# Performance work log

Measured on AMD Instinct MI355X. Metric: run time of the kernel, lower is better.

## Reference

```python
import jax, jax.numpy as jnp
import numpy as np

N_NODES = 50000
N_EDGES = 800000
D = 128
N_REL = 237


def _layer(x, W_I, W_O, rel, b, src, dst):
    # messages over real edges: compose (sub) then project
    msg = (x[src] - rel[edge_safe(dst, None) if False else None] if False else (x[src] - rel_gather)) if False else None
    # (see clean version below)
    raise NotImplementedError


def compgcn_layer(x, W_I, W_O, rel, b, src, dst, etype):
    n = x.shape[0]
    # real edges: gather, compose (sub), project, scatter-add at dst
    msg = (x[src] - rel[etype]) @ W_I.T            # [E, out]
    aggr = jax.ops.segment_sum(msg, dst, num_segments=n)
    # self loops (added with edge_type 0): each node contributes to itself
    self_msg = (x - rel[0]) @ W_I.T                # [N, out]
    # update: aggregated messages + W_O(x) + bias
    return aggr + self_msg + x @ W_O.T + b


def setup_inputs() -> dict:
    key = jax.random.key(0)
    ks = jax.random.split(key, 12)
    x = jax.random.normal(ks[0], (N_NODES, D), dtype=jnp.float32)
    edge_index = jax.random.randint(ks[1], (2, N_EDGES), 0, N_NODES, dtype=jnp.int32)
    edge_type = jax.random.randint(ks[2], (N_EDGES,), 0, N_REL, dtype=jnp.int32)
    def xavier(k, shape):
        bound = float(np.sqrt(6.0 / (shape[0] + shape[1])))
        return jax.random.uniform(k, shape, jnp.float32, -bound, bound)
    return {
        "x": x,
        "edge_index": edge_index,
        "edge_type": edge_type,
        "W_I1": xavier(ks[3], (D, D)), "W_O1": xavier(ks[4], (D, D)),
        "rel1": xavier(ks[5], (N_REL, D)), "b1": jnp.zeros((D,), jnp.float32),
        "W_I2": xavier(ks[6], (D, D)), "W_O2": xavier(ks[7], (D, D)),
        "rel2": xavier(ks[8], (N_REL, D)), "b2": jnp.zeros((D,), jnp.float32),
    }


def reference(x, edge_index, edge_type, W_I1, W_O1, rel1, b1, W_I2, W_O2, rel2, b2):
    src, dst = edge_index[0], edge_index[1]
    h = compgcn_layer(x, W_I1, W_O1, rel1, b1, src, dst, edge_type)
    h = jax.nn.relu(h)  # dropout inactive in eval
    out = compgcn_layer(h, W_I2, W_O2, rel2, b2, src, dst, edge_type)
    return out
```

## Files before the change

### kernel.cpp

```cpp
#include <hip/hip_runtime.h>

#define D 128
#define CAP 3072

typedef __attribute__((ext_vector_type(8))) short short8;
typedef __attribute__((ext_vector_type(4))) float f32x4;

__device__ __forceinline__ float blo(unsigned w) { return __uint_as_float(w << 16); }
__device__ __forceinline__ float bhi(unsigned w) { return __uint_as_float(w & 0xFFFF0000u); }
__device__ __forceinline__ unsigned bpack(float a, float b) {
    unsigned ua = __float_as_uint(a), ub = __float_as_uint(b);
    ua += 0x7FFFu + ((ua >> 16) & 1u);
    ub += 0x7FFFu + ((ub >> 16) & 1u);
    return (ua >> 16) | (ub & 0xFFFF0000u);
}

__global__ __launch_bounds__(256) void setup_mega(
    const float* __restrict__ x,
    const int* __restrict__ srcA, const int* __restrict__ dstA,
    const int* __restrict__ etA,
    const float* __restrict__ WI1, const float* __restrict__ WO1,
    const float* __restrict__ WI2, const float* __restrict__ WO2,
    const float* __restrict__ rel1, const float* __restrict__ rel2,
    const float* __restrict__ b1, const float* __restrict__ b2,
    unsigned* __restrict__ A1,
    unsigned* __restrict__ Wt1, unsigned* __restrict__ Wt2,
    float* __restrict__ c1, float* __restrict__ c2,
    unsigned* __restrict__ rb1, unsigned* __restrict__ rb2,
    int* __restrict__ coarseCnt, unsigned* __restrict__ bulk,
    int N, int E, int relHalf, int nCoarse) {
    int tid = threadIdx.x;
    int bx = blockIdx.x;
    const int B1B = (E + 1023) / 1024;

    if (bx < B1B) {
        __shared__ unsigned pay[1024];
        __shared__ unsigned short ck[1024];
        __shared__ int hist[400];
        __shared__ int base[400];
        int e0 = bx * 1024;
        int cnt = E - e0; if (cnt > 1024) cnt = 1024;
        for (int i = tid; i < nCoarse; i += 256) hist[i] = 0;
        __syncthreads();
        for (int i = tid; i < cnt; i += 256) {
            int e = e0 + i;
            int d = dstA[e];
            pay[i] = (unsigned)srcA[e] | ((unsigned)etA[e] << 17) | ((unsigned)(d & 127) << 25);
            int c = d >> 7;
            ck[i] = (unsigned short)c;
            atomicAdd(&hist[c], 1);
        }
        __syncthreads();
        for (int i = tid; i < nCoarse; i += 256) {
            int h = hist[i];
            base[i] = (h > 0) ? (i * CAP + atomicAdd(&coarseCnt[i], h)) : 0;
            hist[i] = 0;
        }
        __syncthreads();
        for (int i = tid; i < cnt; i += 256) {
            int c = ck[i];
            int pos = base[c] + atomicAdd(&hist[c], 1);
            bulk[pos] = pay[i];
        }
        return;
    }
    bx -= B1B;
    const int CB = (N * 32 + 255) / 256;
    if (bx < CB) {
        int idx = bx * 256 + tid;
        if (idx < N * 32) {
            int n = idx >> 5, q = idx & 31;
            float4 v = ((const float4*)x)[idx];
            uint2 o;
            o.x = bpack(v.x, v.y);
            o.y = bpack(v.z, v.w);
            *(uint2*)(A1 + (size_t)n * 128 + 64 + q * 2) = o;
        }
        return;
    }
    bx -= CB;
    if (bx < 128) {
        int layer = bx >> 6;
        const float* WI = layer ? WI2 : WI1;
        const float* WO = layer ? WO2 : WO1;
        unsigned* Wt = layer ? Wt2 : Wt1;
        int idx = (bx & 63) * 256 + tid;
        int j = idx >> 7;
        int kk = idx & 127;
        int k0 = kk * 2;
        float a, b;
        if (k0 < D) {
            a = WI[j * D + k0];
            b = WI[j * D + k0 + 1];
        } else {
            int kx = k0 - D;
            a = WI[j * D + kx]     + WO[j * D + kx];
            b = WI[j * D + kx + 1] + WO[j * D + kx + 1];
        }
        Wt[idx] = bpack(a, b);
        return;
    }
    bx -= 128;
    if (bx == 0) {
        int layer = tid >> 7;
        int j = tid & (D - 1);
        const float* WI = layer ? WI2 : WI1;
        const float* b  = layer ? b2  : b1;
        const float* rl = layer ? rel2 : rel1;
        float s = b[j];
        for (int k = 0; k < D; ++k) s = fmaf(-WI[j * D + k], rl[k], s);
        (layer ? c2 : c1)[j] = s;
        return;
    }
    bx -= 1;
    {
        int idx = bx * 256 + tid;
        if (idx < 2 * relHalf) {
            const float* src = (idx < relHalf) ? rel1 : rel2;
            unsigned* dst = (idx < relHalf) ? rb1 : rb2;
            int k = (idx < relHalf) ? idx : idx - relHalf;
            float4 v = ((const float4*)src)[k];
            uint2 o;
            o.x = bpack(v.x, v.y);
            o.y = bpack(v.z, v.w);
            *(uint2*)(dst + (size_t)k * 2) = o;
        }
    }
}

__global__ __launch_bounds__(512) void scan_coarse(const int* __restrict__ coarseCnt,
                                                   int* __restrict__ coarseBase,
                                                   int nCoarse, int E) {
    __shared__ int arr[512];
    int tid = threadIdx.x;
    int c = (tid < nCoarse) ? coarseCnt[tid] : 0;
    arr[tid] = c;
    __syncthreads();
    for (int off = 1; off < 512; off <<= 1) {
        int v = (tid >= off) ? arr[tid - off] : 0;
        __syncthreads();
        arr[tid] += v;
        __syncthreads();
    }
    if (tid < nCoarse) coarseBase[tid] = arr[tid] - c;
    if (tid == nCoarse) coarseBase[tid] = E;
}

__global__ __launch_bounds__(256) void bucket2(const unsigned* __restrict__ bulk,
                                               const int* __restrict__ coarseCnt,
                                               const int* __restrict__ coarseBase,
                                               int* __restrict__ row_ptr,
                                               int* __restrict__ col,
                                               int N, int E, int nCoarse) {
    __shared__ unsigned pay[CAP];
    __shared__ int hist[128];
    __shared__ int cur[128];
    int c = blockIdx.x;
    int tid = threadIdx.x;
    int cnt = coarseCnt[c];
    int cb  = coarseBase[c];
    const unsigned* seg = bulk + (size_t)c * CAP;
    if (tid < 128) hist[tid] = 0;
    __syncthreads();
    for (int i = tid; i < cnt; i += 256) {
        unsigned v = seg[i];
        pay[i] = v;
        atomicAdd(&hist[v >> 25], 1);
    }
    __syncthreads();
    int f = tid;
    int myCnt = (f < 128) ? hist[f] : 0;
    for (int off = 1; off < 128; off <<= 1) {
        int v = (f < 128 && f >= off) ? hist[f - off] : 0;
        __syncthreads();
        if (f < 128) hist[f] += v;
        __syncthreads();
    }
    if (f < 128) {
        int excl = hist[f] - myCnt;
        int d = (c << 7) + f;
        if (d < N) row_ptr[d] = cb + excl;
        cur[f] = cb + excl;
    }
    if (c == nCoarse - 1 && tid == 0) row_ptr[N] = E;
    __syncthreads();
    for (int i = tid; i < cnt; i += 256) {
        unsigned v = pay[i];
        int pos = atomicAdd(&cur[v >> 25], 1);
        col[pos] = (int)(v & 0x1FFFFFFu);
    }
}

__global__ __launch_bounds__(256) void gather_kernel(const unsigned* __restrict__ Asrc,
                                                     const int* __restrict__ col,
                                                     const int* __restrict__ row_ptr,
                                                     const unsigned* __restrict__ relb,
                                                     unsigned* __restrict__ Adst, int N) {
    int n = blockIdx.x * 4 + (threadIdx.x >> 6);
    if (n >= N) return;
    int lane = threadIdx.x & 63;
    int g = lane >> 4;
    int h = lane & 15;
    int beg = row_ptr[n];
    int end = row_ptr[n + 1];
    float s[8];
#pragma unroll
    for (int j = 0; j < 8; ++j) s[j] = 0.f;

    for (int base = beg; base < end; base += 64) {
        int ci = base + lane;
        unsigned cv = (unsigned)col[(ci < end) ? ci : beg];
        int m = end - base; if (m > 64) m = 64;
        int e = 0;
        for (; e + 16 <= m; e += 16) {
            uint4 u[4], r[4];
#pragma unroll
            for (int t = 0; t < 4; ++t) {
                unsigned c = (unsigned)__shfl((int)cv, e + 4 * t + g, 64);
                u[t] = ((const uint4*)(Asrc + (size_t)(c & 0x1FFFFu) * 128 + 64))[h];
                r[t] = ((const uint4*)(relb + (size_t)(c >> 17) * 64))[h];
            }
#pragma unroll
            for (int t = 0; t < 4; ++t) {
                s[0] += blo(u[t].x) - blo(r[t].x);
                s[1] += bhi(u[t].x) - bhi(r[t].x);
                s[2] += blo(u[t].y) - blo(r[t].y);
                s[3] += bhi(u[t].y) - bhi(r[t].y);
                s[4] += blo(u[t].z) - blo(r[t].z);
                s[5] += bhi(u[t].z) - bhi(r[t].z);
                s[6] += blo(u[t].w) - blo(r[t].w);
                s[7] += bhi(u[t].w) - bhi(r[t].w);
            }
        }
        for (; e + 4 <= m; e += 4) {
            unsigned c = (unsigned)__shfl((int)cv, e + g, 64);
            uint4 u = ((const uint4*)(Asrc + (size_t)(c & 0x1FFFFu) * 128 + 64))[h];
            uint4 r = ((const uint4*)(relb + (size_t)(c >> 17) * 64))[h];
            s[0] += blo(u.x) - blo(r.x);
            s[1] += bhi(u.x) - bhi(r.x);
            s[2] += blo(u.y) - blo(r.y);
            s[3] += bhi(u.y) - bhi(r.y);
            s[4] += blo(u.z) - blo(r.z);
            s[5] += bhi(u.z) - bhi(r.z);
            s[6] += blo(u.w) - blo(r.w);
            s[7] += bhi(u.w) - bhi(r.w);
        }
        if (e < m) {
            int idx = e + g;
            unsigned c = (unsigned)__shfl((int)cv, (idx < m) ? idx : 0, 64);
            if (idx < m) {
                uint4 u = ((const uint4*)(Asrc + (size_t)(c & 0x1FFFFu) * 128 + 64))[h];
                uint4 r = ((const uint4*)(relb + (size_t)(c >> 17) * 64))[h];
                s[0] += blo(u.x) - blo(r.x);
                s[1] += bhi(u.x) - bhi(r.x);
                s[2] += blo(u.y) - blo(r.y);
                s[3] += bhi(u.y) - bhi(r.y);
                s[4] += blo(u.z) - blo(r.z);
                s[5] += bhi(u.z) - bhi(r.z);
                s[6] += blo(u.w) - blo(r.w);
                s[7] += bhi(u.w) - bhi(r.w);
            }
        }
    }
#pragma unroll
    for (int j = 0; j < 8; ++j) {
        s[j] += __shfl_xor(s[j], 16, 64);
        s[j] += __shfl_xor(s[j], 32, 64);
    }
    if (g == 0) {
        uint4 o;
        o.x = bpack(s[0], s[1]);
        o.y = bpack(s[2], s[3]);
        o.z = bpack(s[4], s[5]);
        o.w = bpack(s[6], s[7]);
        ((uint4*)(Adst + (size_t)n * 128))[h] = o;
    }
}

__global__ __launch_bounds__(256) void node_mfma(
    const unsigned* A,
    const unsigned* __restrict__ Wt,
    const float* __restrict__ cvec,
    float* outf,
    unsigned* __restrict__ outb,
    int do_relu, int N) {
    __shared__ unsigned WtS[128 * 32];
    __shared__ unsigned AS[128 * 32];
    int tid = threadIdx.x;
    int w = tid >> 6;
    int lane = tid & 63;
    int m = lane & 15;
    int quad = lane >> 4;
    int nbase = blockIdx.x * 128;

    f32x4 acc[2][8];
#pragma unroll
    for (int nt = 0; nt < 2; ++nt)
#pragma unroll
        for (int t = 0; t < 8; ++t) acc[nt][t] = (f32x4)(0.f);

    for (int kc = 0; kc < 4; ++kc) {
        for (int i = tid; i < 1024; i += 256) {
            int j = i >> 3, q = i & 7;
            uint4 v = ((const uint4*)Wt)[j * 32 + kc * 8 + q];
            *(uint4*)&WtS[j * 32 + 4 * (q ^ (j & 7))] = v;
        }
        for (int i = tid; i < 1024; i += 256) {
            int n = i >> 3, q = i & 7;
            int gn = nbase + n;
            uint4 v = make_uint4(0u, 0u, 0u, 0u);
            if (gn < N) v = ((const uint4*)A)[(size_t)gn * 32 + kc * 8 + q];
            *(uint4*)&AS[n * 32 + 4 * (q ^ (n & 7))] = v;
        }
        __syncthreads();

#pragma unroll
        for (int s = 0; s < 2; ++s) {
            int g = s * 4 + quad;
            int r0 = w * 32 + m;
            int r1 = r0 + 16;
            short8 b0 = *(const short8*)&AS[r0 * 32 + 4 * (g ^ (r0 & 7))];
            short8 b1 = *(const short8*)&AS[r1 * 32 + 4 * (g ^ (r1 & 7))];
#pragma unroll
            for (int t = 0; t < 8; ++t) {
                int jr = t * 16 + m;
                short8 a = *(const short8*)&WtS[jr * 32 + 4 * (g ^ (jr & 7))];
                acc[0][t] = __builtin_amdgcn_mfma_f32_16x16x32_bf16(a, b0, acc[0][t], 0, 0, 0);
                acc[1][t] = __builtin_amdgcn_mfma_f32_16x16x32_bf16(a, b1, acc[1][t], 0, 0, 0);
            }
        }
        __syncthreads();
    }

#pragma unroll
    for (int nt = 0; nt < 2; ++nt) {
        int node = nbase + w * 32 + nt * 16 + m;
        if (node < N) {
#pragma unroll
            for (int t = 0; t < 8; ++t) {
                float4 cv = ((const float4*)cvec)[t * 4 + quad];
                f32x4 a = acc[nt][t];
                float v0 = a[0] + cv.x;
                float v1 = a[1] + cv.y;
                float v2 = a[2] + cv.z;
                float v3 = a[3] + cv.w;
                if (do_relu) {
                    v0 = fmaxf(v0, 0.f); v1 = fmaxf(v1, 0.f);
                    v2 = fmaxf(v2, 0.f); v3 = fmaxf(v3, 0.f);
                }
                if (outf) {
                    ((float4*)outf)[(size_t)node * 32 + t * 4 + quad] =
                        make_float4(v0, v1, v2, v3);
                } else {
                    uint2 o;
                    o.x = bpack(v0, v1);
                    o.y = bpack(v2, v3);
                    ((uint2*)(outb + (size_t)node * 128))[32 + t * 4 + quad] = o;
                }
            }
        }
    }
}

extern "C" void kernel_launch(void* const* d_in, const int* in_sizes, int n_in,
                              void* d_out, int out_size, void* d_ws, size_t ws_size,
                              hipStream_t stream) {
    const float* x    = (const float*)d_in[0];
    const int*   ei   = (const int*)d_in[1];
    const int*   et   = (const int*)d_in[2];
    const float* WI1  = (const float*)d_in[3];
    const float* WO1  = (const float*)d_in[4];
    const float* rel1 = (const float*)d_in[5];
    const float* b1   = (const float*)d_in[6];
    const float* WI2  = (const float*)d_in[7];
    const float* WO2  = (const float*)d_in[8];
    const float* rel2 = (const float*)d_in[9];
    const float* b2   = (const float*)d_in[10];

    const int E = in_sizes[2];
    const int N = in_sizes[0] / D;
    const int* src = ei;
    const int* dst = ei + E;
    const int nCoarse = (N + 127) / 128;

    unsigned* wsu  = (unsigned*)d_ws;
    unsigned* A1   = wsu;
    unsigned* Wt1  = A1 + (size_t)N * 128;
    unsigned* Wt2  = Wt1 + 16384;
    float*    cvec1 = (float*)(Wt2 + 16384);
    float*    cvec2 = cvec1 + D;
    unsigned* rb1  = (unsigned*)(cvec2 + D);
    unsigned* rb2  = rb1 + 237 * 64;
    int*      coarseCnt  = (int*)(rb2 + 237 * 64);
    int*      coarseBase = coarseCnt + 512;
    int*      row_ptr    = coarseBase + 512;
    int*      col        = row_ptr + N + 4;
    unsigned* bulk       = (unsigned*)(col + E);

    unsigned* A2 = (unsigned*)d_out;

    const int relHalf = 237 * 32;
    const int B1B = (E + 1023) / 1024;
    const int CB = (N * 32 + 255) / 256;
    const int RB = (2 * relHalf + 255) / 256;

    hipMemsetAsync(coarseCnt, 0, 512 * sizeof(int), stream);
    setup_mega<<<B1B + CB + 128 + 1 + RB, 256, 0, stream>>>(
        x, src, dst, et, WI1, WO1, WI2, WO2, rel1, rel2, b1, b2,
        A1, Wt1, Wt2, cvec1, cvec2, rb1, rb2,
        coarseCnt, bulk, N, E, relHalf, nCoarse);

    scan_coarse<<<1, 512, 0, stream>>>(coarseCnt, coarseBase, nCoarse, E);
    bucket2<<<nCoarse, 256, 0, stream>>>(bulk, coarseCnt, coarseBase,
                                         row_ptr, col, N, E, nCoarse);

    const int gather_blocks = (N + 3) / 4;
    const int node_blocks = (N + 127) / 128;

    gather_kernel<<<gather_blocks, 256, 0, stream>>>(A1, col, row_ptr, rb1, A1, N);
    node_mfma<<<node_blocks, 256, 0, stream>>>(A1, Wt1, cvec1,
                                               (float*)nullptr, A2, 1, N);

    gather_kernel<<<gather_blocks, 256, 0, stream>>>(A2, col, row_ptr, rb2, A2, N);
    node_mfma<<<node_blocks, 256, 0, stream>>>(A2, Wt2, cvec2,
                                               (float*)d_out, (unsigned*)nullptr, 0, N);
}
```

Baseline: 247.0 us.

## Replace two-level bucket CSR build with degree histogram, prefix scan and atomic scatter

Builds the destination-sorted CSR by counting per-node degrees with global atomics, computing row pointers per 128-node chunk with a redundant block-local prefix sum, then scattering packed src/etype entries through per-node atomic cursors. This removes the intermediate bulk buffer, the coarse scan kernel and the shared-memory bucket pass. In exchange it uses many scattered global atomics, and each rowptr block re-reduces the whole degree prefix, which is quadratic in the number of chunks. The order of entries within a row is no longer deterministic.

```diff
diff --git a/kernel.cpp b/kernel.cpp
--- a/kernel.cpp
+++ b/kernel.cpp
@@ -1,7 +1,6 @@
 #include <hip/hip_runtime.h>
 
 #define D 128
-#define CAP 3072
 
 typedef __attribute__((ext_vector_type(8))) short short8;
 typedef __attribute__((ext_vector_type(4))) float f32x4;
@@ -17,8 +16,7 @@
 
 __global__ __launch_bounds__(256) void setup_mega(
     const float* __restrict__ x,
-    const int* __restrict__ srcA, const int* __restrict__ dstA,
-    const int* __restrict__ etA,
+    const int* __restrict__ dstA,
     const float* __restrict__ WI1, const float* __restrict__ WO1,
     const float* __restrict__ WI2, const float* __restrict__ WO2,
     const float* __restrict__ rel1, const float* __restrict__ rel2,
@@ -27,44 +25,31 @@
     unsigned* __restrict__ Wt1, unsigned* __restrict__ Wt2,
     float* __restrict__ c1, float* __restrict__ c2,
     unsigned* __restrict__ rb1, unsigned* __restrict__ rb2,
-    int* __restrict__ coarseCnt, unsigned* __restrict__ bulk,
-    int N, int E, int relHalf, int nCoarse) {
+    int* __restrict__ degree,
+    int N, int E, int relHalf) {
     int tid = threadIdx.x;
     int bx = blockIdx.x;
-    const int B1B = (E + 1023) / 1024;
-
-    if (bx < B1B) {
-        __shared__ unsigned pay[1024];
-        __shared__ unsigned short ck[1024];
-        __shared__ int hist[400];
-        __shared__ int base[400];
-        int e0 = bx * 1024;
-        int cnt = E - e0; if (cnt > 1024) cnt = 1024;
-        for (int i = tid; i < nCoarse; i += 256) hist[i] = 0;
-        __syncthreads();
-        for (int i = tid; i < cnt; i += 256) {
-            int e = e0 + i;
-            int d = dstA[e];
-            pay[i] = (unsigned)srcA[e] | ((unsigned)etA[e] << 17) | ((unsigned)(d & 127) << 25);
-            int c = d >> 7;
-            ck[i] = (unsigned short)c;
-            atomicAdd(&hist[c], 1);
-        }
-        __syncthreads();
-        for (int i = tid; i < nCoarse; i += 256) {
-            int h = hist[i];
-            base[i] = (h > 0) ? (i * CAP + atomicAdd(&coarseCnt[i], h)) : 0;
-            hist[i] = 0;
-        }
-        __syncthreads();
-        for (int i = tid; i < cnt; i += 256) {
-            int c = ck[i];
-            int pos = base[c] + atomicAdd(&hist[c], 1);
-            bulk[pos] = pay[i];
+    const int HB = (E + 4095) / 4096;
+
+    if (bx < HB) {
+        int base = bx * 4096;
+#pragma unroll
+        for (int r = 0; r < 4; ++r) {
+            int e = base + r * 1024 + tid * 4;
+            if (e + 4 <= E) {
+                int4 d = *(const int4*)(dstA + e);
+                atomicAdd(&degree[d.x], 1);
+                atomicAdd(&degree[d.y], 1);
+                atomicAdd(&degree[d.z], 1);
+                atomicAdd(&degree[d.w], 1);
+            } else {
+                for (int k = e; k < E && k < e + 4; ++k)
+                    atomicAdd(&degree[dstA[k]], 1);
+            }
         }
         return;
     }
-    bx -= B1B;
+    bx -= HB;
     const int CB = (N * 32 + 255) / 256;
     if (bx < CB) {
         int idx = bx * 256 + tid;
@@ -128,66 +113,75 @@
     }
 }
 
-__global__ __launch_bounds__(512) void scan_coarse(const int* __restrict__ coarseCnt,
-                                                   int* __restrict__ coarseBase,
-                                                   int nCoarse, int E) {
-    __shared__ int arr[512];
-    int tid = threadIdx.x;
-    int c = (tid < nCoarse) ? coarseCnt[tid] : 0;
-    arr[tid] = c;
-    __syncthreads();
-    for (int off = 1; off < 512; off <<= 1) {
-        int v = (tid >= off) ? arr[tid - off] : 0;
-        __syncthreads();
-        arr[tid] += v;
-        __syncthreads();
-    }
-    if (tid < nCoarse) coarseBase[tid] = arr[tid] - c;
-    if (tid == nCoarse) coarseBase[tid] = E;
-}
-
-__global__ __launch_bounds__(256) void bucket2(const unsigned* __restrict__ bulk,
-                                               const int* __restrict__ coarseCnt,
-                                               const int* __restrict__ coarseBase,
-                                               int* __restrict__ row_ptr,
-                                               int* __restrict__ col,
-                                               int N, int E, int nCoarse) {
-    __shared__ unsigned pay[CAP];
-    __shared__ int hist[128];
-    __shared__ int cur[128];
+__global__ __launch_bounds__(256) void rowptr_kernel(const int* __restrict__ degree,
+                                                     int* __restrict__ row_ptr,
+                                                     int* __restrict__ cur,
+                                                     int N, int E, int nCoarse) {
+    __shared__ int red[256];
+    __shared__ int sc[128];
     int c = blockIdx.x;
     int tid = threadIdx.x;
-    int cnt = coarseCnt[c];
-    int cb  = coarseBase[c];
-    const unsigned* seg = bulk + (size_t)c * CAP;
-    if (tid < 128) hist[tid] = 0;
+    int lim = c * 128;
+    int s = 0;
+    for (int i = tid * 4; i < lim; i += 1024) {
+        int4 v = *(const int4*)(degree + i);
+        s += v.x + v.y + v.z + v.w;
+    }
+    red[tid] = s;
     __syncthreads();
-    for (int i = tid; i < cnt; i += 256) {
-        unsigned v = seg[i];
-        pay[i] = v;
-        atomicAdd(&hist[v >> 25], 1);
+    for (int off = 128; off > 0; off >>= 1) {
+        if (tid < off) red[tid] += red[tid + off];
+        __syncthreads();
+    }
+    int base = red[0];
+    int f = tid;
+    int d = 0;
+    if (f < 128) {
+        int node = lim + f;
+        d = (node < N) ? degree[node] : 0;
+        sc[f] = d;
     }
     __syncthreads();
-    int f = tid;
-    int myCnt = (f < 128) ? hist[f] : 0;
     for (int off = 1; off < 128; off <<= 1) {
-        int v = (f < 128 && f >= off) ? hist[f - off] : 0;
+        int v = (f < 128 && f >= off) ? sc[f - off] : 0;
         __syncthreads();
-        if (f < 128) hist[f] += v;
+        if (f < 128) sc[f] += v;
         __syncthreads();
     }
     if (f < 128) {
-        int excl = hist[f] - myCnt;
-        int d = (c << 7) + f;
-        if (d < N) row_ptr[d] = cb + excl;
-        cur[f] = cb + excl;
+        int node = lim + f;
+        if (node < N) {
+            int rp = base + sc[f] - d;
+            row_ptr[node] = rp;
+            cur[node] = rp;
+        }
     }
     if (c == nCoarse - 1 && tid == 0) row_ptr[N] = E;
-    __syncthreads();
-    for (int i = tid; i < cnt; i += 256) {
-        unsigned v = pay[i];
-        int pos = atomicAdd(&cur[v >> 25], 1);
-        col[pos] = (int)(v & 0x1FFFFFFu);
+}
+
+__global__ __launch_bounds__(256) void scatter_kernel(const int* __restrict__ srcA,
+                                                      const int* __restrict__ dstA,
+                                                      const int* __restrict__ etA,
+                                                      int* __restrict__ cur,
+                                                      int* __restrict__ col, int E) {
+    int e = (blockIdx.x * 256 + threadIdx.x) * 4;
+    if (e + 4 <= E) {
+        int4 s4 = *(const int4*)(srcA + e);
+        int4 d4 = *(const int4*)(dstA + e);
+        int4 t4 = *(const int4*)(etA + e);
+        int p0 = atomicAdd(&cur[d4.x], 1);
+        int p1 = atomicAdd(&cur[d4.y], 1);
+        int p2 = atomicAdd(&cur[d4.z], 1);
+        int p3 = atomicAdd(&cur[d4.w], 1);
+        col[p0] = s4.x | (t4.x << 17);
+        col[p1] = s4.y | (t4.y << 17);
+        col[p2] = s4.z | (t4.z << 17);
+        col[p3] = s4.w | (t4.w << 17);
+    } else {
+        for (int k = e; k < E && k < e + 4; ++k) {
+            int p = atomicAdd(&cur[dstA[k]], 1);
+            col[p] = srcA[k] | (etA[k] << 17);
+        }
     }
 }
 
@@ -391,28 +385,26 @@
     float*    cvec2 = cvec1 + D;
     unsigned* rb1  = (unsigned*)(cvec2 + D);
     unsigned* rb2  = rb1 + 237 * 64;
-    int*      coarseCnt  = (int*)(rb2 + 237 * 64);
-    int*      coarseBase = coarseCnt + 512;
-    int*      row_ptr    = coarseBase + 512;
-    int*      col        = row_ptr + N + 4;
-    unsigned* bulk       = (unsigned*)(col + E);
+    int*      degree = (int*)(rb2 + 237 * 64);
+    int*      cur    = degree + 51200;
+    int*      row_ptr = cur + 51200;
+    int*      col     = row_ptr + N + 16;
 
     unsigned* A2 = (unsigned*)d_out;
 
     const int relHalf = 237 * 32;
-    const int B1B = (E + 1023) / 1024;
+    const int HB = (E + 4095) / 4096;
     const int CB = (N * 32 + 255) / 256;
     const int RB = (2 * relHalf + 255) / 256;
 
-    hipMemsetAsync(coarseCnt, 0, 512 * sizeof(int), stream);
-    setup_mega<<<B1B + CB + 128 + 1 + RB, 256, 0, stream>>>(
-        x, src, dst, et, WI1, WO1, WI2, WO2, rel1, rel2, b1, b2,
+    hipMemsetAsync(degree, 0, 51200 * sizeof(int), stream);
+    setup_mega<<<HB + CB + 128 + 1 + RB, 256, 0, stream>>>(
+        x, dst, WI1, WO1, WI2, WO2, rel1, rel2, b1, b2,
         A1, Wt1, Wt2, cvec1, cvec2, rb1, rb2,
-        coarseCnt, bulk, N, E, relHalf, nCoarse);
-
-    scan_coarse<<<1, 512, 0, stream>>>(coarseCnt, coarseBase, nCoarse, E);
-    bucket2<<<nCoarse, 256, 0, stream>>>(bulk, coarseCnt, coarseBase,
-                                         row_ptr, col, N, E, nCoarse);
+        degree, N, E, relHalf);
+
+    rowptr_kernel<<<nCoarse, 256, 0, stream>>>(degree, row_ptr, cur, N, E, nCoarse);
+    scatter_kernel<<<(E + 1023) / 1024, 256, 0, stream>>>(src, dst, et, cur, col, E);
 
     const int gather_blocks = (N + 3) / 4;
     const int node_blocks = (N + 127) / 128;
```

After: 291.1 us. 17.9% more time.
